# Performance work log

Hardware: AMD Instinct MI355X
Metric: run time of the kernel (lower is better)

Reference implementation:

```python
import jax, jax.numpy as jnp
import numpy as np

S = 64    # shapelets_size
N = 256   # num_shapelets
C = 3     # in_channels
B = 64
L = 2048


def setup_inputs() -> dict:
    key = jax.random.key(0)
    kx, ks = jax.random.split(key)
    x = jax.random.normal(kx, (B, C, L), dtype=jnp.float32)
    shapelets = jax.random.normal(ks, (C, N, S), dtype=jnp.float32)
    return {"x": x, "shapelets": shapelets}


def reference(x, shapelets):
    # x: (B, C, L); shapelets: (C, N, S)
    W = x.shape[2] - S + 1  # number of sliding windows
    # unfold: (B, C, W, S)
    idx = jnp.arange(W)[:, None] + jnp.arange(S)[None, :]
    win = x[:, :, idx]
    # cdist with mm-based euclidean: d^2 = |a|^2 + |b|^2 - 2 a.b
    win_sq = jnp.sum(win * win, axis=-1)                 # (B, C, W)
    shp_sq = jnp.sum(shapelets * shapelets, axis=-1)     # (C, N)
    cross = jnp.einsum('bcws,cns->bcwn', win, shapelets)  # (B, C, W, N)
    d2 = win_sq[..., None] + shp_sq[None, :, None, :] - 2.0 * cross
    d = jnp.sqrt(jnp.maximum(d2, 0.0))                   # (B, C, W, N)
    # sum over channels, keepdim -> (B, 1, W, N); transpose -> (B, 1, N, W); min over W
    summed = jnp.sum(d, axis=1, keepdims=True)
    out = jnp.min(jnp.swapaxes(summed, 2, 3), axis=3)    # (B, 1, N)
    return out
```

## Files before the change

kernel.cpp:

```cpp
#include <hip/hip_runtime.h>
#include <hip/hip_fp16.h>


typedef float  v4f __attribute__((ext_vector_type(4)));
typedef short  v8s __attribute__((ext_vector_type(8)));
typedef unsigned short u16;
typedef unsigned int   u32;
typedef unsigned long long u64;

#define S_ 64
#define N_ 256
#define C_ 3
#define B_ 64
#define L_ 2048
#define W_ 1985
#define NCHUNK 530
#define THREADS 512
#define WAVES 8

__device__ __forceinline__ u16 f2bf(float f) {
    u32 u = __builtin_bit_cast(u32, f);
    return (u16)((u + 0x7FFFu + ((u >> 16) & 1u)) >> 16);
}
__device__ __forceinline__ float bf2f(u16 b) {
    return __builtin_bit_cast(float, ((u32)b) << 16);
}

__global__ __launch_bounds__(THREADS, 2)
void shapelet_min_kernel(const float* __restrict__ x,
                         const float* __restrict__ shp,
                         float* __restrict__ out)
{
    __shared__ u64 xcopy[C_][4][NCHUNK];
    __shared__ __half wsq[C_][L_];
    __shared__ float red[WAVES][64];

    const int tid  = threadIdx.x;
    const int wave = tid >> 6;
    const int lane = tid & 63;
    const int m    = lane & 15;
    const int q    = lane >> 4;
    const int b    = blockIdx.x >> 2;
    const int n0   = (blockIdx.x & 3) << 6;

    u16* scratch = (u16*)&xcopy[0][0][0];
    #pragma unroll
    for (int k = 0; k < 6; ++k) {
        int idx = tid + k * THREADS;
        int sq = idx & 15;
        int n  = (idx >> 4) & 63;
        int c  = idx >> 10;
        v4f v = *(const v4f*)(shp + ((size_t)(c * N_ + n0 + n) * S_ + (sq << 2)));
        u64 pk = (u64)f2bf(v[0]) | ((u64)f2bf(v[1]) << 16)
               | ((u64)f2bf(v[2]) << 32) | ((u64)f2bf(v[3]) << 48);
        *(u64*)(scratch + ((c * 64 + n) * 72 + (sq << 2))) = pk;
    }
    __syncthreads();

    v8s bfr[C_][4][2];
    float ssq[C_][4];
    #pragma unroll
    for (int c = 0; c < C_; ++c) {
        #pragma unroll
        for (int nt = 0; nt < 4; ++nt) {
            float sacc = 0.f;
            #pragma unroll
            for (int h = 0; h < 2; ++h) {
                v8s f = *(const v8s*)(scratch + ((c * 64 + nt * 16 + m) * 72 + h * 32 + q * 8));
                bfr[c][nt][h] = f;
                #pragma unroll
                for (int j = 0; j < 8; ++j) {
                    float e = bf2f((u16)f[j]);
                    sacc += e * e;
                }
            }
            sacc += __shfl_xor(sacc, 16);
            sacc += __shfl_xor(sacc, 32);
            ssq[c][nt] = sacc;
        }
    }
    __syncthreads();

    {
        const float* xb = x + (size_t)b * (C_ * L_);
        #pragma unroll
        for (int k = 0; k < 4; ++k) {
            int gi = tid + k * THREADS;
            if (gi < C_ * NCHUNK) {
                int c = gi / NCHUNK;
                int t = gi - c * NCHUNK;
                int e = t << 2;
                float f[4];
                if (e + 3 < L_) {
                    v4f v = *(const v4f*)(xb + c * L_ + e);
                    f[0] = v[0]; f[1] = v[1]; f[2] = v[2]; f[3] = v[3];
                } else {
                    #pragma unroll
                    for (int i = 0; i < 4; ++i)
                        f[i] = (e + i < L_) ? xb[c * L_ + e + i] : 0.f;
                }
                u16 u[4];
                #pragma unroll
                for (int i = 0; i < 4; ++i) u[i] = f2bf(f[i]);
                #pragma unroll
                for (int r = 0; r < 4; ++r) {
                    u16* cp = (u16*)&xcopy[c][r][0];
                    #pragma unroll
                    for (int i = 0; i < 4; ++i) {
                        int pos = e + i - r;
                        if (pos >= 0) cp[pos] = u[i];
                    }
                }
            }
        }
    }
    __syncthreads();

    #pragma unroll
    for (int c = 0; c < C_; ++c) {
        const u64* cp0 = &xcopy[c][0][0];
        float e[68];
        #pragma unroll
        for (int kk = 0; kk < 17; ++kk) {
            u64 ch = cp0[tid + kk];
            e[kk * 4 + 0] = bf2f((u16)(ch));
            e[kk * 4 + 1] = bf2f((u16)(ch >> 16));
            e[kk * 4 + 2] = bf2f((u16)(ch >> 32));
            e[kk * 4 + 3] = bf2f((u16)(ch >> 48));
        }
        float s0 = 0.f;
        #pragma unroll
        for (int i = 0; i < 64; ++i) s0 += e[i] * e[i];
        float s1 = s0 - e[0] * e[0] + e[64] * e[64];
        float s2 = s1 - e[1] * e[1] + e[65] * e[65];
        float s3 = s2 - e[2] * e[2] + e[66] * e[66];
        union { u64 u; __half h[4]; } hp;
        hp.h[0] = __float2half(s0); hp.h[1] = __float2half(s1);
        hp.h[2] = __float2half(s2); hp.h[3] = __float2half(s3);
        *(u64*)&wsq[c][tid << 2] = hp.u;
    }
    __syncthreads();

    float mins[4] = {1e30f, 1e30f, 1e30f, 1e30f};
    const int r = m & 3;

    #pragma unroll 1
    for (int it = 0; it < 8; ++it) {
        const int wbase = it * 256 + wave * 32;
        if (wbase >= W_) continue;

        float sums[2][4][4];
        #pragma unroll
        for (int mt = 0; mt < 2; ++mt)
            #pragma unroll
            for (int nt = 0; nt < 4; ++nt)
                #pragma unroll
                for (int g = 0; g < 4; ++g) sums[mt][nt][g] = 0.f;

        #pragma unroll
        for (int c = 0; c < C_; ++c) {
            v8s afr[2][2];
            #pragma unroll
            for (int mt = 0; mt < 2; ++mt) {
                #pragma unroll
                for (int h = 0; h < 2; ++h) {
                    int p0 = wbase + mt * 16 + m + h * 32 + q * 8;
                    int T  = (p0 - r) >> 2;
                    const u64* cp = &xcopy[c][r][0];
                    union { u64 u[2]; v8s v; } tmp;
                    tmp.u[0] = cp[T];
                    tmp.u[1] = cp[T + 1];
                    afr[mt][h] = tmp.v;
                }
            }
            v4f acc[2][4];
            #pragma unroll
            for (int mt = 0; mt < 2; ++mt)
                #pragma unroll
                for (int nt = 0; nt < 4; ++nt)
                    acc[mt][nt] = (v4f){0.f, 0.f, 0.f, 0.f};

            #pragma unroll
            for (int h = 0; h < 2; ++h)
                #pragma unroll
                for (int mt = 0; mt < 2; ++mt)
                    #pragma unroll
                    for (int nt = 0; nt < 4; ++nt)
                        acc[mt][nt] = __builtin_amdgcn_mfma_f32_16x16x32_bf16(
                            afr[mt][h], bfr[c][nt][h], acc[mt][nt], 0, 0, 0);

            #pragma unroll
            for (int mt = 0; mt < 2; ++mt) {
                union { u64 u; __half h4[4]; } wq;
                wq.u = *(const u64*)&wsq[c][wbase + mt * 16 + q * 4];
                float wv[4];
                #pragma unroll
                for (int g = 0; g < 4; ++g) wv[g] = __half2float(wq.h4[g]);
                #pragma unroll
                for (int nt = 0; nt < 4; ++nt) {
                    #pragma unroll
                    for (int g = 0; g < 4; ++g) {
                        float d2 = wv[g] + ssq[c][nt] - 2.f * acc[mt][nt][g];
                        d2 = fmaxf(d2, 0.f);
                        sums[mt][nt][g] += __builtin_amdgcn_sqrtf(d2);
                    }
                }
            }
        }
        #pragma unroll
        for (int mt = 0; mt < 2; ++mt) {
            #pragma unroll
            for (int g = 0; g < 4; ++g) {
                int w = wbase + mt * 16 + q * 4 + g;
                bool ok = (w < W_);
                #pragma unroll
                for (int nt = 0; nt < 4; ++nt) {
                    float vv = ok ? sums[mt][nt][g] : 1e30f;
                    mins[nt] = fminf(mins[nt], vv);
                }
            }
        }
    }

    #pragma unroll
    for (int nt = 0; nt < 4; ++nt) {
        mins[nt] = fminf(mins[nt], __shfl_xor(mins[nt], 16));
        mins[nt] = fminf(mins[nt], __shfl_xor(mins[nt], 32));
    }
    if (lane < 16) {
        #pragma unroll
        for (int nt = 0; nt < 4; ++nt) red[wave][nt * 16 + lane] = mins[nt];
    }
    __syncthreads();
    if (tid < 64) {
        float v = red[0][tid];
        #pragma unroll
        for (int wv = 1; wv < WAVES; ++wv) v = fminf(v, red[wv][tid]);
        out[(size_t)b * N_ + n0 + tid] = v;
    }
}

extern "C" void kernel_launch(void* const* d_in, const int* in_sizes, int n_in,
                              void* d_out, int out_size, void* d_ws, size_t ws_size,
                              hipStream_t stream) {
    const float* x   = (const float*)d_in[0];
    const float* shp = (const float*)d_in[1];
    float* out       = (float*)d_out;
    hipLaunchKernelGGL(shapelet_min_kernel, dim3(256), dim3(THREADS), 0, stream,
                       x, shp, out);
}
```

Measured before the change: 84.62 us.

## Split windows and shapelets across more blocks with atomicMin reduction

The grid grows fourfold by splitting the window range in two and shrinking each block's shapelet tile to 32. Partial minima are combined with an atomicMin on float bits, after a separate init kernel sets outputs to infinity. The squared-norm terms are pre-scaled by -0.5 and used to seed the MFMA accumulator, which removes the per-element epilogue arithmetic. The cost is an extra kernel launch, duplicated x staging per block, and less reuse of A fragments.

```diff
diff --git a/kernel.cpp b/kernel.cpp
--- a/kernel.cpp
+++ b/kernel.cpp
@@ -11,12 +11,12 @@
 #define S_ 64
 #define N_ 256
 #define C_ 3
-#define B_ 64
 #define L_ 2048
 #define W_ 1985
-#define NCHUNK 530
-#define THREADS 512
-#define WAVES 8
+#define WL 1024
+#define NCH 274
+#define THREADS 256
+#define OUT_ELEMS 16384
 
 __device__ __forceinline__ u16 f2bf(float f) {
     u32 u = __builtin_bit_cast(u32, f);
@@ -26,47 +26,55 @@
     return __builtin_bit_cast(float, ((u32)b) << 16);
 }
 
-__global__ __launch_bounds__(THREADS, 2)
+__global__ __launch_bounds__(256)
+void init_out_kernel(u32* __restrict__ out_u) {
+    int i = blockIdx.x * 256 + threadIdx.x;
+    if (i < OUT_ELEMS) out_u[i] = 0x7F800000u;
+}
+
+__global__ __launch_bounds__(THREADS, 4)
 void shapelet_min_kernel(const float* __restrict__ x,
                          const float* __restrict__ shp,
-                         float* __restrict__ out)
+                         u32* __restrict__ out_u)
 {
-    __shared__ u64 xcopy[C_][4][NCHUNK];
-    __shared__ __half wsq[C_][L_];
-    __shared__ float red[WAVES][64];
+    __shared__ u64 xcopy[C_][4][NCH];
+    __shared__ __half hwq[C_][WL];
 
     const int tid  = threadIdx.x;
     const int wave = tid >> 6;
     const int lane = tid & 63;
     const int m    = lane & 15;
     const int q    = lane >> 4;
-    const int b    = blockIdx.x >> 2;
-    const int n0   = (blockIdx.x & 3) << 6;
+    const int wh   = blockIdx.x & 1;
+    const int nb   = (blockIdx.x >> 1) & 7;
+    const int b    = blockIdx.x >> 4;
+    const int n0   = nb << 5;
+    const int wstart = wh * WL;
 
     u16* scratch = (u16*)&xcopy[0][0][0];
     #pragma unroll
     for (int k = 0; k < 6; ++k) {
         int idx = tid + k * THREADS;
         int sq = idx & 15;
-        int n  = (idx >> 4) & 63;
-        int c  = idx >> 10;
+        int n  = (idx >> 4) & 31;
+        int c  = idx >> 9;
         v4f v = *(const v4f*)(shp + ((size_t)(c * N_ + n0 + n) * S_ + (sq << 2)));
         u64 pk = (u64)f2bf(v[0]) | ((u64)f2bf(v[1]) << 16)
                | ((u64)f2bf(v[2]) << 32) | ((u64)f2bf(v[3]) << 48);
-        *(u64*)(scratch + ((c * 64 + n) * 72 + (sq << 2))) = pk;
-    }
-    __syncthreads();
-
-    v8s bfr[C_][4][2];
-    float ssq[C_][4];
+        *(u64*)(scratch + ((c * 32 + n) * 72 + (sq << 2))) = pk;
+    }
+    __syncthreads();
+
+    v8s   bfr[C_][2][2];
+    float hs[C_][2];
     #pragma unroll
     for (int c = 0; c < C_; ++c) {
         #pragma unroll
-        for (int nt = 0; nt < 4; ++nt) {
+        for (int nt = 0; nt < 2; ++nt) {
             float sacc = 0.f;
             #pragma unroll
             for (int h = 0; h < 2; ++h) {
-                v8s f = *(const v8s*)(scratch + ((c * 64 + nt * 16 + m) * 72 + h * 32 + q * 8));
+                v8s f = *(const v8s*)(scratch + ((c * 32 + nt * 16 + m) * 72 + h * 32 + q * 8));
                 bfr[c][nt][h] = f;
                 #pragma unroll
                 for (int j = 0; j < 8; ++j) {
@@ -76,7 +84,7 @@
             }
             sacc += __shfl_xor(sacc, 16);
             sacc += __shfl_xor(sacc, 32);
-            ssq[c][nt] = sacc;
+            hs[c][nt] = -0.5f * sacc;
         }
     }
     __syncthreads();
@@ -86,18 +94,19 @@
         #pragma unroll
         for (int k = 0; k < 4; ++k) {
             int gi = tid + k * THREADS;
-            if (gi < C_ * NCHUNK) {
-                int c = gi / NCHUNK;
-                int t = gi - c * NCHUNK;
+            if (gi < C_ * NCH) {
+                int c = gi / NCH;
+                int t = gi - c * NCH;
                 int e = t << 2;
+                int ge = wstart + e;
                 float f[4];
-                if (e + 3 < L_) {
-                    v4f v = *(const v4f*)(xb + c * L_ + e);
+                if (ge + 3 < L_) {
+                    v4f v = *(const v4f*)(xb + c * L_ + ge);
                     f[0] = v[0]; f[1] = v[1]; f[2] = v[2]; f[3] = v[3];
                 } else {
                     #pragma unroll
                     for (int i = 0; i < 4; ++i)
-                        f[i] = (e + i < L_) ? xb[c * L_ + e + i] : 0.f;
+                        f[i] = (ge + i < L_) ? xb[c * L_ + ge + i] : 0.f;
                 }
                 u16 u[4];
                 #pragma unroll
@@ -135,86 +144,77 @@
         float s2 = s1 - e[1] * e[1] + e[65] * e[65];
         float s3 = s2 - e[2] * e[2] + e[66] * e[66];
         union { u64 u; __half h[4]; } hp;
-        hp.h[0] = __float2half(s0); hp.h[1] = __float2half(s1);
-        hp.h[2] = __float2half(s2); hp.h[3] = __float2half(s3);
-        *(u64*)&wsq[c][tid << 2] = hp.u;
-    }
-    __syncthreads();
-
-    float mins[4] = {1e30f, 1e30f, 1e30f, 1e30f};
-    const int r = m & 3;
+        hp.h[0] = __float2half(-0.5f * s0); hp.h[1] = __float2half(-0.5f * s1);
+        hp.h[2] = __float2half(-0.5f * s2); hp.h[3] = __float2half(-0.5f * s3);
+        *(u64*)&hwq[c][tid << 2] = hp.u;
+    }
+    __syncthreads();
+
+    float mins[2] = {1e30f, 1e30f};
 
     #pragma unroll 1
     for (int it = 0; it < 8; ++it) {
-        const int wbase = it * 256 + wave * 32;
-        if (wbase >= W_) continue;
-
-        float sums[2][4][4];
+        const int wb = it * 128 + wave * 32;
+        if (wstart + wb >= W_) continue;
+
+        float sums[2][2][4];
         #pragma unroll
         for (int mt = 0; mt < 2; ++mt)
             #pragma unroll
-            for (int nt = 0; nt < 4; ++nt)
+            for (int nt = 0; nt < 2; ++nt)
                 #pragma unroll
                 for (int g = 0; g < 4; ++g) sums[mt][nt][g] = 0.f;
 
         #pragma unroll
         for (int c = 0; c < C_; ++c) {
-            v8s afr[2][2];
+            v4f acc[2][2];
             #pragma unroll
             for (int mt = 0; mt < 2; ++mt) {
-                #pragma unroll
-                for (int h = 0; h < 2; ++h) {
-                    int p0 = wbase + mt * 16 + m + h * 32 + q * 8;
+                union { u64 u; __half h4[4]; } wq;
+                wq.u = *(const u64*)&hwq[c][wb + mt * 16 + q * 4];
+                #pragma unroll
+                for (int g = 0; g < 4; ++g) {
+                    float hv = __half2float(wq.h4[g]);
+                    acc[mt][0][g] = hv + hs[c][0];
+                    acc[mt][1][g] = hv + hs[c][1];
+                }
+            }
+            #pragma unroll
+            for (int h = 0; h < 2; ++h) {
+                v8s afr[2];
+                #pragma unroll
+                for (int mt = 0; mt < 2; ++mt) {
+                    int p0 = wb + mt * 16 + m + h * 32 + q * 8;
+                    int r  = m & 3;
                     int T  = (p0 - r) >> 2;
                     const u64* cp = &xcopy[c][r][0];
                     union { u64 u[2]; v8s v; } tmp;
                     tmp.u[0] = cp[T];
                     tmp.u[1] = cp[T + 1];
-                    afr[mt][h] = tmp.v;
-                }
-            }
-            v4f acc[2][4];
+                    afr[mt] = tmp.v;
+                }
+                #pragma unroll
+                for (int mt = 0; mt < 2; ++mt)
+                    #pragma unroll
+                    for (int nt = 0; nt < 2; ++nt)
+                        acc[mt][nt] = __builtin_amdgcn_mfma_f32_16x16x32_bf16(
+                            afr[mt], bfr[c][nt][h], acc[mt][nt], 0, 0, 0);
+            }
             #pragma unroll
             for (int mt = 0; mt < 2; ++mt)
                 #pragma unroll
-                for (int nt = 0; nt < 4; ++nt)
-                    acc[mt][nt] = (v4f){0.f, 0.f, 0.f, 0.f};
-
-            #pragma unroll
-            for (int h = 0; h < 2; ++h)
-                #pragma unroll
-                for (int mt = 0; mt < 2; ++mt)
-                    #pragma unroll
-                    for (int nt = 0; nt < 4; ++nt)
-                        acc[mt][nt] = __builtin_amdgcn_mfma_f32_16x16x32_bf16(
-                            afr[mt][h], bfr[c][nt][h], acc[mt][nt], 0, 0, 0);
-
-            #pragma unroll
-            for (int mt = 0; mt < 2; ++mt) {
-                union { u64 u; __half h4[4]; } wq;
-                wq.u = *(const u64*)&wsq[c][wbase + mt * 16 + q * 4];
-                float wv[4];
-                #pragma unroll
-                for (int g = 0; g < 4; ++g) wv[g] = __half2float(wq.h4[g]);
-                #pragma unroll
-                for (int nt = 0; nt < 4; ++nt) {
-                    #pragma unroll
-                    for (int g = 0; g < 4; ++g) {
-                        float d2 = wv[g] + ssq[c][nt] - 2.f * acc[mt][nt][g];
-                        d2 = fmaxf(d2, 0.f);
-                        sums[mt][nt][g] += __builtin_amdgcn_sqrtf(d2);
-                    }
-                }
-            }
+                for (int nt = 0; nt < 2; ++nt)
+                    #pragma unroll
+                    for (int g = 0; g < 4; ++g)
+                        sums[mt][nt][g] += __builtin_amdgcn_sqrtf(fmaxf(-acc[mt][nt][g], 0.f));
         }
         #pragma unroll
         for (int mt = 0; mt < 2; ++mt) {
             #pragma unroll
             for (int g = 0; g < 4; ++g) {
-                int w = wbase + mt * 16 + q * 4 + g;
-                bool ok = (w < W_);
-                #pragma unroll
-                for (int nt = 0; nt < 4; ++nt) {
+                bool ok = (wstart + wb + mt * 16 + q * 4 + g) < W_;
+                #pragma unroll
+                for (int nt = 0; nt < 2; ++nt) {
                     float vv = ok ? sums[mt][nt][g] : 1e30f;
                     mins[nt] = fminf(mins[nt], vv);
                 }
@@ -223,20 +223,16 @@
     }
 
     #pragma unroll
-    for (int nt = 0; nt < 4; ++nt) {
+    for (int nt = 0; nt < 2; ++nt) {
         mins[nt] = fminf(mins[nt], __shfl_xor(mins[nt], 16));
         mins[nt] = fminf(mins[nt], __shfl_xor(mins[nt], 32));
     }
     if (lane < 16) {
         #pragma unroll
-        for (int nt = 0; nt < 4; ++nt) red[wave][nt * 16 + lane] = mins[nt];
-    }
-    __syncthreads();
-    if (tid < 64) {
-        float v = red[0][tid];
-        #pragma unroll
-        for (int wv = 1; wv < WAVES; ++wv) v = fminf(v, red[wv][tid]);
-        out[(size_t)b * N_ + n0 + tid] = v;
+        for (int nt = 0; nt < 2; ++nt) {
+            float v = mins[nt] * 1.41421356237f;
+            atomicMin(out_u + ((size_t)b * N_ + n0 + nt * 16 + m), __float_as_uint(v));
+        }
     }
 }
 
@@ -245,7 +241,9 @@
                               hipStream_t stream) {
     const float* x   = (const float*)d_in[0];
     const float* shp = (const float*)d_in[1];
-    float* out       = (float*)d_out;
-    hipLaunchKernelGGL(shapelet_min_kernel, dim3(256), dim3(THREADS), 0, stream,
-                       x, shp, out);
-}
+    u32* out_u       = (u32*)d_out;
+
+    hipLaunchKernelGGL(init_out_kernel, dim3((OUT_ELEMS + 255) / 256), dim3(256), 0, stream, out_u);
+    hipLaunchKernelGGL(shapelet_min_kernel, dim3(1024), dim3(THREADS), 0, stream,
+                       x, (const float*)shp, out_u);
+}
```

Measured after the change: 92.26 us. 9.0% more time.
